# Performance work log

Hardware: AMD Instinct MI355X
Metric: run time of the kernel (lower is better)

## Reference

```python
import jax, jax.numpy as jnp
import numpy as np

NE, NR, D, H, L = 200000, 500, 128, 4, 2
HD = D // H
N, E, B = 32768, 262144, 256
MARGIN = 1.0


def setup_inputs() -> dict:
    key = jax.random.key(0)
    ks = jax.random.split(key, 16)
    nrm = lambda k, shp, s=0.05: jax.random.normal(k, shp, jnp.float32) * s
    inp = {
        'ent_emb': nrm(ks[0], (NE, D)),
        'rel_emb': nrm(ks[1], (NR, D)),
        'rel_prior': nrm(ks[2], (NR, 1)),
    }
    for i, nm in enumerate(['Wq', 'Wk', 'Wv', 'Wo', 'Wek', 'Wev']):
        inp[nm] = nrm(ks[3 + i], (L, D, D))
    for gi, g in enumerate(['h', 't', 'n']):
        kb = jax.random.fold_in(key, 100 + gi)
        k1, k2, k3, k4 = jax.random.split(kb, 4)
        inp[f'x_{g}'] = jax.random.randint(k1, (N,), 0, NE, jnp.int32)
        inp[f'ei_{g}'] = jax.random.randint(k2, (2, E), 0, N, jnp.int32)
        inp[f'ea_{g}'] = jax.random.randint(k3, (E,), 0, NR, jnp.int32)
        inp[f'y_{g}'] = jax.random.randint(k4, (B,), 0, N // B, jnp.int32)
        inp[f's_{g}'] = jnp.full((B,), N // B, dtype=jnp.int32)
    inp['sample'] = jax.random.randint(ks[9], (B, 3), 0, NR, jnp.int32)
    return inp


def gnn_embed(ent_emb, rel_emb, rel_prior, Wq, Wk, Wv, Wo, Wek, Wev, x, ei, ea, y, s):
    n = x.shape[0]
    h = ent_emb[x]                    # [N, D] node features (embedding lookup)
    e_emb = rel_emb[ea]               # [E, D] edge relation embedding
    e_pri = rel_prior[ea]             # [E, 1] scalar relation prior gate
    src, dst = ei[0], ei[1]
    scale = 1.0 / np.sqrt(HD).astype(np.float32)
    for l in range(L):
        q = (h @ Wq[l]).reshape(n, H, HD)[dst]                               # [E,H,HD]
        k = (h @ Wk[l]).reshape(n, H, HD)[src] + (e_emb @ Wek[l]).reshape(-1, H, HD)
        v = (h @ Wv[l]).reshape(n, H, HD)[src] + (e_emb @ Wev[l]).reshape(-1, H, HD)
        score = jnp.sum(q * k, axis=-1) * scale * e_pri                      # [E,H]
        # segment softmax over incoming edges of each destination node
        m = jax.ops.segment_max(score, dst, num_segments=n)
        m = jnp.where(jnp.isfinite(m), m, 0.0)
        ex = jnp.exp(score - m[dst])
        den = jax.ops.segment_sum(ex, dst, num_segments=n)[dst]
        alpha = ex / (den + 1e-16)                                           # [E,H]
        msg = jax.ops.segment_sum((alpha[..., None] * v).reshape(-1, D), dst, num_segments=n)
        h = jax.nn.gelu(h + msg @ Wo[l])                                     # residual + activation
    # get_real_index: exclusive cumsum of graph sizes + local target index
    offsets = jnp.concatenate([jnp.zeros((1,), s.dtype), jnp.cumsum(s)[:-1]])
    return h[offsets + y]             # [B, D]


def reference(ent_emb, rel_emb, rel_prior, Wq, Wk, Wv, Wo, Wek, Wev,
              x_h, ei_h, ea_h, y_h, s_h,
              x_t, ei_t, ea_t, y_t, s_t,
              x_n, ei_n, ea_n, y_n, s_n, sample):
    g = lambda x, ei, ea, y, s: gnn_embed(ent_emb, rel_emb, rel_prior, Wq, Wk, Wv, Wo, Wek, Wev, x, ei, ea, y, s)
    h = g(x_h, ei_h, ea_h, y_h, s_h)[:, None, :]   # [B,1,D]
    t = g(x_t, ei_t, ea_t, y_t, s_t)[:, None, :]
    tn = g(x_n, ei_n, ea_n, y_n, s_n)[:, None, :]
    r = rel_emb[sample[:, 1]][:, None, :]          # [B,1,D]
    proj_t = h + r                                 # TransE projection
    pos = jnp.linalg.norm(t - proj_t + 1e-8, axis=2)   # [B,1]
    negs = jnp.linalg.norm(t - tn + 1e-8, axis=2)      # [B,1]
    neg = jnp.mean(negs, axis=-1)                      # [B]
    # MarginRankingLoss(pos, neg, target=-1): mean(max(0, (pos-neg)+margin)); broadcasts [B,1]-[B] -> [B,B]
    loss = jnp.mean(jnp.maximum(pos - neg + MARGIN, 0.0))
    return loss
```

## Files before the change

### kernel.cpp

```cpp
#include <hip/hip_runtime.h>
#include <hip/hip_bf16.h>
#include <math.h>

#define NEC 200000
#define NRC 500
#define DD 128
#define LLC 2
#define NNODE 32768
#define EEDGE 262144
#define BBATCH 256
#define NG 3
#define BCAP 32

typedef __attribute__((ext_vector_type(8))) short short8;
typedef __attribute__((ext_vector_type(4))) float floatx4;
typedef __attribute__((ext_vector_type(2))) float floatx2;

__device__ __forceinline__ float bf2f(unsigned short u) {
  union { unsigned int i; float f; } c; c.i = ((unsigned int)u) << 16; return c.f;
}
__device__ __forceinline__ unsigned short f2bf(float f) {
  union { float f; unsigned int i; } c; c.f = f;
  unsigned int x = c.i;
  unsigned int r = x + 0x7fffu + ((x >> 16) & 1u);
  return (unsigned short)(r >> 16);
}
__device__ __forceinline__ float bfu_lo(unsigned int u) {
  union { unsigned int i; float f; } c; c.i = u << 16; return c.f;
}
__device__ __forceinline__ float bfu_hi(unsigned int u) {
  union { unsigned int i; float f; } c; c.i = u & 0xffff0000u; return c.f;
}

__device__ __forceinline__ bool detect_fm(const void* ent) {
  unsigned int u = ((const unsigned int*)ent)[threadIdx.x & 63];
  bool big = fabsf(bfu_lo(u)) > 100.f;
  return __ballot(big) != 0ull;
}

__global__ __launch_bounds__(128) void k_prep(const void* ent, const void* rel,
    const void* prior, const void* Wq, const void* Wk, const void* Wv, const void* Wo,
    const void* Wek, const void* Wev,
    float* pris, unsigned short* WT, unsigned short* relk, unsigned short* relv, int* deg) {
  bool fm = detect_fm(ent);
  int bid = blockIdx.x, tid = threadIdx.x;
  if (bid < 4) {
    int r = bid * 128 + tid;
    if (r < NRC) {
      float p = fm ? ((const float*)prior)[r] : bf2f(((const unsigned short*)prior)[r]);
      pris[r] = p * 0.17677669529663687f;
    }
  } else if (bid < 1028) {
    int t = (bid - 4) * 128 + tid;
    int mat = t >> 15;
    int rem = t & 32767;
    int l = rem >> 14;
    int p = rem & 16383;
    int d = p >> 7, c = p & 127;
    const void* W = mat == 0 ? Wq : (mat == 1 ? Wk : (mat == 2 ? Wv : Wo));
    size_t src = (size_t)l * DD * DD + (size_t)c * DD + d;
    float v = fm ? ((const float*)W)[src] : bf2f(((const unsigned short*)W)[src]);
    WT[(((size_t)mat * LLC + l) * DD + d) * DD + c] = f2bf(v);
  } else if (bid < 3028) {
    int rid = bid - 1028;
    int which = rid / 1000;
    int l = (rid / 500) % 2;
    int r = rid % 500;
    int d = tid;
    size_t wofs = (size_t)l * DD * DD;
    const float* Wf = (const float*)(which ? Wev : Wek) + wofs;
    const unsigned short* Wb = (const unsigned short*)(which ? Wev : Wek) + wofs;
    __shared__ float re[DD];
    re[d] = fm ? ((const float*)rel)[r * DD + d] : bf2f(((const unsigned short*)rel)[r * DD + d]);
    __syncthreads();
    float acc = 0.f;
    if (fm) { for (int c = 0; c < DD; ++c) acc += re[c] * Wf[c * DD + d]; }
    else    { for (int c = 0; c < DD; ++c) acc += re[c] * bf2f(Wb[c * DD + d]); }
    unsigned short* out = which ? relv : relk;
    out[((size_t)l * NRC + r) * DD + d] = f2bf(acc);
  } else {
    int t = (bid - 3028) * 128 + tid;
    uint4 z = {0u, 0u, 0u, 0u};
    ((uint4*)deg)[t * 2] = z;
    ((uint4*)deg)[t * 2 + 1] = z;
  }
}

__global__ __launch_bounds__(256) void k_gb(const void* ent,
    const int* x0, const int* x1, const int* x2,
    const int* ei0, const int* ea0, const int* ei1, const int* ea1,
    const int* ei2, const int* ea2,
    unsigned short* hbf, int* deg, unsigned int* bucket) {
  int bid = blockIdx.x, tid = threadIdx.x;
  if (bid < 3072) {
    bool fm = detect_fm(ent);
    int rbase = bid * 32;
    int g = rbase >> 15;
    const int* x = g == 0 ? x0 : (g == 1 ? x1 : x2);
    int c = tid & 31;
    int j4 = tid >> 5;
    int rows[4], xs[4];
    #pragma unroll
    for (int k = 0; k < 4; ++k) {
      rows[k] = rbase + j4 + 8 * k;
      xs[k] = x[rows[k] & (NNODE - 1)];
    }
    if (fm) {
      float4 v[4];
      #pragma unroll
      for (int k = 0; k < 4; ++k)
        v[k] = *reinterpret_cast<const float4*>((const float*)ent + (size_t)xs[k] * DD + c * 4);
      #pragma unroll
      for (int k = 0; k < 4; ++k) {
        uint2 o;
        o.x = ((unsigned int)f2bf(v[k].y) << 16) | (unsigned int)f2bf(v[k].x);
        o.y = ((unsigned int)f2bf(v[k].w) << 16) | (unsigned int)f2bf(v[k].z);
        *reinterpret_cast<uint2*>(hbf + (size_t)rows[k] * DD + c * 4) = o;
      }
    } else {
      uint2 v[4];
      #pragma unroll
      for (int k = 0; k < 4; ++k)
        v[k] = *reinterpret_cast<const uint2*>((const unsigned short*)ent + (size_t)xs[k] * DD + c * 4);
      #pragma unroll
      for (int k = 0; k < 4; ++k)
        *reinterpret_cast<uint2*>(hbf + (size_t)rows[k] * DD + c * 4) = v[k];
    }
  } else {
    int bb = bid - 3072;
    int g = bb >> 8;
    const int* ei = g == 0 ? ei0 : (g == 1 ? ei1 : ei2);
    const int* ea = g == 0 ? ea0 : (g == 1 ? ea1 : ea2);
    int e0 = (bb & 255) * 1024 + tid * 4;
    uint4 d4 = *reinterpret_cast<const uint4*>(ei + EEDGE + e0);
    uint4 s4 = *reinterpret_cast<const uint4*>(ei + e0);
    uint4 r4 = *reinterpret_cast<const uint4*>(ea + e0);
    int* degg = deg + g * NNODE;
    size_t brow = (size_t)g * NNODE;
    #pragma unroll
    for (int k = 0; k < 4; ++k) {
      int dst = (int)((const unsigned int*)&d4)[k];
      unsigned int src = ((const unsigned int*)&s4)[k];
      unsigned int r = ((const unsigned int*)&r4)[k];
      int pos = atomicAdd(&degg[dst], 1);
      if (pos < BCAP)
        bucket[(brow + dst) * BCAP + pos] = src | (r << 15);
    }
  }
}

__device__ __forceinline__ void stage_wt(const unsigned short* WT, int tid,
                                         unsigned short (*Wt)[136]) {
  #pragma unroll
  for (int pass = 0; pass < 8; ++pass) {
    int idx = pass * 256 + tid;
    int d = idx >> 4, c0 = (idx & 15) << 3;
    *reinterpret_cast<short8*>(&Wt[d][c0]) =
        *reinterpret_cast<const short8*>(WT + d * DD + c0);
  }
}

__global__ __launch_bounds__(256) void k_gemm_qkv(const unsigned short* A,
    const unsigned short* WT, int layer, unsigned short* Qo, unsigned char* KV) {
  __shared__ unsigned short Wt[DD][136];
  int mat = blockIdx.y;
  int g = blockIdx.z;
  const unsigned short* Ag = A + (size_t)g * NNODE * DD;
  int tid = threadIdx.x;
  stage_wt(WT + ((size_t)mat * LLC + layer) * DD * DD, tid, Wt);
  __syncthreads();
  int w = tid >> 6, lane = tid & 63;
  int m = lane & 15, quad = lane >> 4;
  int row = blockIdx.x * 64 + w * 16 + m;
  floatx4 acc[8];
  #pragma unroll
  for (int t = 0; t < 8; ++t) acc[t] = (floatx4){0.f, 0.f, 0.f, 0.f};
  const unsigned short* arow = Ag + (size_t)row * DD;
  #pragma unroll
  for (int ks = 0; ks < 4; ++ks) {
    short8 a = *reinterpret_cast<const short8*>(arow + ks * 32 + quad * 8);
    #pragma unroll
    for (int t = 0; t < 8; ++t) {
      short8 b = *reinterpret_cast<const short8*>(&Wt[t * 16 + m][ks * 32 + quad * 8]);
      acc[t] = __builtin_amdgcn_mfma_f32_16x16x32_bf16(a, b, acc[t], 0, 0, 0);
    }
  }
  __syncthreads();
  unsigned short* ut = &Wt[0][0];
  #pragma unroll
  for (int t = 0; t < 8; ++t) {
    #pragma unroll
    for (int r = 0; r < 4; ++r) {
      ut[(w * 16 + quad * 4 + r) * 136 + t * 16 + m] = f2bf(acc[t][r]);
    }
  }
  __syncthreads();
  int rowbase = blockIdx.x * 64;
  if (mat == 0) {
    unsigned short* Og = Qo + (size_t)g * NNODE * DD;
    #pragma unroll
    for (int k = 0; k < 4; ++k) {
      int flat = k * 256 + tid;
      int rw = flat >> 4, c8 = flat & 15;
      short8 v = *reinterpret_cast<const short8*>(ut + rw * 136 + c8 * 8);
      *reinterpret_cast<short8*>(Og + (size_t)(rowbase + rw) * DD + c8 * 8) = v;
    }
  } else {
    unsigned char* kvb = KV + (size_t)g * NNODE * 256 + (mat == 1 ? 0 : 128);
    #pragma unroll
    for (int k = 0; k < 2; ++k) {
      int flat = k * 256 + tid;
      int rw = flat >> 3, c16 = flat & 7;
      const unsigned short* p = ut + rw * 136 + c16 * 16;
      uint4 a = *reinterpret_cast<const uint4*>(p);
      uint4 b = *reinterpret_cast<const uint4*>(p + 8);
      unsigned int w0 = __builtin_amdgcn_cvt_pk_fp8_f32(bfu_lo(a.x), bfu_hi(a.x), 0u, false);
      w0 = __builtin_amdgcn_cvt_pk_fp8_f32(bfu_lo(a.y), bfu_hi(a.y), w0, true);
      unsigned int w1 = __builtin_amdgcn_cvt_pk_fp8_f32(bfu_lo(a.z), bfu_hi(a.z), 0u, false);
      w1 = __builtin_amdgcn_cvt_pk_fp8_f32(bfu_lo(a.w), bfu_hi(a.w), w1, true);
      unsigned int w2 = __builtin_amdgcn_cvt_pk_fp8_f32(bfu_lo(b.x), bfu_hi(b.x), 0u, false);
      w2 = __builtin_amdgcn_cvt_pk_fp8_f32(bfu_lo(b.y), bfu_hi(b.y), w2, true);
      unsigned int w3 = __builtin_amdgcn_cvt_pk_fp8_f32(bfu_lo(b.z), bfu_hi(b.z), 0u, false);
      w3 = __builtin_amdgcn_cvt_pk_fp8_f32(bfu_lo(b.w), bfu_hi(b.w), w3, true);
      uint4 o = {w0, w1, w2, w3};
      *reinterpret_cast<uint4*>(kvb + (size_t)(rowbase + rw) * 256 + c16 * 16) = o;
    }
  }
}

__global__ __launch_bounds__(256) void k_gemm_o(const unsigned short* A,
    const unsigned short* WT, int layer, unsigned short* hbf) {
  __shared__ unsigned short Wt[DD][136];
  int g = blockIdx.y;
  const unsigned short* Ag = A + (size_t)g * NNODE * DD;
  unsigned short* hbg = hbf + (size_t)g * NNODE * DD;
  int tid = threadIdx.x;
  stage_wt(WT + ((size_t)3 * LLC + layer) * DD * DD, tid, Wt);
  __syncthreads();
  int w = tid >> 6, lane = tid & 63;
  int m = lane & 15, quad = lane >> 4;
  int row = blockIdx.x * 64 + w * 16 + m;
  floatx4 acc[8];
  #pragma unroll
  for (int t = 0; t < 8; ++t) acc[t] = (floatx4){0.f, 0.f, 0.f, 0.f};
  const unsigned short* arow = Ag + (size_t)row * DD;
  #pragma unroll
  for (int ks = 0; ks < 4; ++ks) {
    short8 a = *reinterpret_cast<const short8*>(arow + ks * 32 + quad * 8);
    #pragma unroll
    for (int t = 0; t < 8; ++t) {
      short8 b = *reinterpret_cast<const short8*>(&Wt[t * 16 + m][ks * 32 + quad * 8]);
      acc[t] = __builtin_amdgcn_mfma_f32_16x16x32_bf16(a, b, acc[t], 0, 0, 0);
    }
  }
  __syncthreads();
  float* ft = (float*)&Wt[0][0];
  #pragma unroll
  for (int t = 0; t < 8; ++t) {
    #pragma unroll
    for (int r = 0; r < 4; ++r) {
      ft[(w * 16 + quad * 4 + r) * 136 + t * 16 + m] = acc[t][r];
    }
  }
  __syncthreads();
  int rowbase = blockIdx.x * 64;
  #pragma unroll
  for (int k = 0; k < 8; ++k) {
    int flat = k * 256 + tid;
    int rw = flat >> 5, c4 = flat & 31;
    float4 v = *reinterpret_cast<const float4*>(ft + rw * 136 + c4 * 4);
    size_t gi = (size_t)(rowbase + rw) * DD + c4 * 4;
    uint2 hv = *reinterpret_cast<const uint2*>(hbg + gi);
    float h0 = bfu_lo(hv.x), h1 = bfu_hi(hv.x), h2 = bfu_lo(hv.y), h3 = bfu_hi(hv.y);
    float r0, r1, r2, r3;
    {
      float xv = v.x + h0;
      float z2 = 1.5957691216057308f * (xv + 0.044715f * xv * xv * xv);
      r0 = xv / (1.f + __expf(-z2));
      xv = v.y + h1;
      z2 = 1.5957691216057308f * (xv + 0.044715f * xv * xv * xv);
      r1 = xv / (1.f + __expf(-z2));
      xv = v.z + h2;
      z2 = 1.5957691216057308f * (xv + 0.044715f * xv * xv * xv);
      r2 = xv / (1.f + __expf(-z2));
      xv = v.w + h3;
      z2 = 1.5957691216057308f * (xv + 0.044715f * xv * xv * xv);
      r3 = xv / (1.f + __expf(-z2));
    }
    uint2 o;
    o.x = ((unsigned int)f2bf(r1) << 16) | (unsigned int)f2bf(r0);
    o.y = ((unsigned int)f2bf(r3) << 16) | (unsigned int)f2bf(r2);
    *reinterpret_cast<uint2*>(hbg + gi) = o;
  }
}

__global__ __launch_bounds__(256) void k_attn(const unsigned short* Q, const unsigned char* KV,
    const unsigned short* relk, const unsigned short* relv,
    const float* pris, const int* deg, const unsigned int* bucket, int layer,
    unsigned short* msgb) {
  int w = threadIdx.x >> 6, lane = threadIdx.x & 63;
  int half = lane >> 5;
  int hq = (lane >> 4) & 1;
  int sl = lane & 15;
  int g = blockIdx.y;
  int dst = blockIdx.x * 8 + w * 2 + half;
  const unsigned short* rk = relk + (size_t)layer * NRC * DD;
  const unsigned short* rv = relv + (size_t)layer * NRC * DD;
  const unsigned char* KVg = KV + (size_t)g * NNODE * 256;
  size_t gofs = (size_t)g * NNODE * DD;

  uint4 qu = *reinterpret_cast<const uint4*>(Q + gofs + (size_t)dst * DD + sl * 8);
  float q0 = bfu_lo(qu.x), q1 = bfu_hi(qu.x), q2 = bfu_lo(qu.y), q3 = bfu_hi(qu.y);
  float q4 = bfu_lo(qu.z), q5 = bfu_hi(qu.z), q6 = bfu_lo(qu.w), q7 = bfu_hi(qu.w);

  float den = 0.f;
  float m0 = 0.f, m1 = 0.f, m2 = 0.f, m3 = 0.f, m4 = 0.f, m5 = 0.f, m6 = 0.f, m7 = 0.f;
  int dg = deg[g * NNODE + dst]; if (dg > BCAP) dg = BCAP;
  size_t base = ((size_t)g * NNODE + dst) * BCAP;
  if (dg > 0) {
    int niter = (dg + 1) >> 1;
    unsigned int pe = bucket[base + (hq < dg ? hq : dg - 1)];
    for (int i = 0; i < niter; ++i) {
      unsigned int cur = pe;
      int nx = 2 * (i + 1) + hq; if (nx >= dg) nx = dg - 1;
      pe = bucket[base + nx];
      int src = (int)(cur & 32767u);
      int r = (int)(cur >> 15);
      const unsigned char* kvrow = KVg + (size_t)src * 256;
      uint2 k8 = *reinterpret_cast<const uint2*>(kvrow + sl * 8);
      uint2 v8 = *reinterpret_cast<const uint2*>(kvrow + 128 + sl * 8);
      uint4 rku = *reinterpret_cast<const uint4*>(rk + (size_t)r * DD + sl * 8);
      uint4 rvu = *reinterpret_cast<const uint4*>(rv + (size_t)r * DD + sl * 8);
      float p = pris[r];
      floatx2 k01 = __builtin_amdgcn_cvt_pk_f32_fp8(k8.x, false);
      floatx2 k23 = __builtin_amdgcn_cvt_pk_f32_fp8(k8.x, true);
      floatx2 k45 = __builtin_amdgcn_cvt_pk_f32_fp8(k8.y, false);
      floatx2 k67 = __builtin_amdgcn_cvt_pk_f32_fp8(k8.y, true);
      float s = q0 * (k01.x + bfu_lo(rku.x))
              + q1 * (k01.y + bfu_hi(rku.x))
              + q2 * (k23.x + bfu_lo(rku.y))
              + q3 * (k23.y + bfu_hi(rku.y))
              + q4 * (k45.x + bfu_lo(rku.z))
              + q5 * (k45.y + bfu_hi(rku.z))
              + q6 * (k67.x + bfu_lo(rku.w))
              + q7 * (k67.y + bfu_hi(rku.w));
      s += __shfl_xor(s, 1); s += __shfl_xor(s, 2);
      bool valid = (2 * i + hq) < dg;
      float ex = valid ? __expf(s * p) : 0.f;
      floatx2 v01 = __builtin_amdgcn_cvt_pk_f32_fp8(v8.x, false);
      floatx2 v23 = __builtin_amdgcn_cvt_pk_f32_fp8(v8.x, true);
      floatx2 v45 = __builtin_amdgcn_cvt_pk_f32_fp8(v8.y, false);
      floatx2 v67 = __builtin_amdgcn_cvt_pk_f32_fp8(v8.y, true);
      den += ex;
      m0 += ex * (v01.x + bfu_lo(rvu.x));
      m1 += ex * (v01.y + bfu_hi(rvu.x));
      m2 += ex * (v23.x + bfu_lo(rvu.y));
      m3 += ex * (v23.y + bfu_hi(rvu.y));
      m4 += ex * (v45.x + bfu_lo(rvu.z));
      m5 += ex * (v45.y + bfu_hi(rvu.z));
      m6 += ex * (v67.x + bfu_lo(rvu.w));
      m7 += ex * (v67.y + bfu_hi(rvu.w));
    }
  }
  den += __shfl_xor(den, 16);
  m0 += __shfl_xor(m0, 16);
  m1 += __shfl_xor(m1, 16);
  m2 += __shfl_xor(m2, 16);
  m3 += __shfl_xor(m3, 16);
  m4 += __shfl_xor(m4, 16);
  m5 += __shfl_xor(m5, 16);
  m6 += __shfl_xor(m6, 16);
  m7 += __shfl_xor(m7, 16);
  float inv = 1.f / (den + 1e-16f);
  if (hq == 0) {
    uint4 o;
    o.x = ((unsigned int)f2bf(m1 * inv) << 16) | (unsigned int)f2bf(m0 * inv);
    o.y = ((unsigned int)f2bf(m3 * inv) << 16) | (unsigned int)f2bf(m2 * inv);
    o.z = ((unsigned int)f2bf(m5 * inv) << 16) | (unsigned int)f2bf(m4 * inv);
    o.w = ((unsigned int)f2bf(m7 * inv) << 16) | (unsigned int)f2bf(m6 * inv);
    *reinterpret_cast<uint4*>(msgb + gofs + (size_t)dst * DD + sl * 8) = o;
  }
}

__global__ __launch_bounds__(128) void k_ep(const unsigned short* hbf, const void* ent,
    const void* rel,
    const int* y0, const int* s0, const int* y1, const int* s1, const int* y2, const int* s2,
    const int* sample, float* pos, float* neg) {
  bool fm = detect_fm(ent);
  int b = blockIdx.x, d = threadIdx.x;
  int oh = 0, ot = 0, on = 0;
  for (int j = 0; j < b; ++j) { oh += s0[j]; ot += s1[j]; on += s2[j]; }
  int ih = oh + y0[b], it = ot + y1[b], in_ = on + y2[b];
  float th = bf2f(hbf[((size_t)0 * NNODE + ih) * DD + d]);
  float tt = bf2f(hbf[((size_t)1 * NNODE + it) * DD + d]);
  float tn = bf2f(hbf[((size_t)2 * NNODE + in_) * DD + d]);
  int r = sample[b * 3 + 1];
  float rr = fm ? ((const float*)rel)[r * DD + d] : bf2f(((const unsigned short*)rel)[r * DD + d]);
  float dp = tt - (th + rr) + 1e-8f;
  float dn = tt - tn + 1e-8f;
  float ap = dp * dp, an = dn * dn;
  for (int o = 32; o > 0; o >>= 1) { ap += __shfl_down(ap, o); an += __shfl_down(an, o); }
  __shared__ float sa[2], sb[2];
  if ((d & 63) == 0) { sa[d >> 6] = ap; sb[d >> 6] = an; }
  __syncthreads();
  if (d == 0) { pos[b] = sqrtf(sa[0] + sa[1]); neg[b] = sqrtf(sb[0] + sb[1]); }
}

__global__ __launch_bounds__(256) void k_hinge(const float* pos, const float* neg,
    const void* ent, void* out) {
  bool fm = detect_fm(ent);
  __shared__ float ns[BBATCH];
  __shared__ float wsum[4];
  int t = threadIdx.x;
  ns[t] = neg[t];
  float pb = pos[t];
  __syncthreads();
  float local = 0.f;
  for (int j = 0; j < BBATCH; ++j) {
    float v = pb - ns[j] + 1.0f;
    local += v > 0.f ? v : 0.f;
  }
  for (int o = 32; o > 0; o >>= 1) local += __shfl_down(local, o);
  if ((t & 63) == 0) wsum[t >> 6] = local;
  __syncthreads();
  if (t == 0) {
    float loss = (wsum[0] + wsum[1] + wsum[2] + wsum[3]) * (1.f / (256.f * 256.f));
    if (fm) ((float*)out)[0] = loss;
    else    ((unsigned short*)out)[0] = f2bf(loss);
  }
}

extern "C" void kernel_launch(void* const* d_in, const int* in_sizes, int n_in,
                              void* d_out, int out_size, void* d_ws, size_t ws_size,
                              hipStream_t stream) {
  const void* ent   = d_in[0];
  const void* rel   = d_in[1];
  const void* prior = d_in[2];
  const void* Wq  = d_in[3];
  const void* Wk  = d_in[4];
  const void* Wv  = d_in[5];
  const void* Wo  = d_in[6];
  const void* Wek = d_in[7];
  const void* Wev = d_in[8];
  const int* sample = (const int*)d_in[24];

  size_t off = 0;
  char* basep = (char*)d_ws;
  auto alloc = [&](size_t bytes) -> void* {
    void* r = basep + off;
    off = (off + bytes + 255) & ~(size_t)255;
    return r;
  };
  unsigned short* hbf  = (unsigned short*)alloc((size_t)NG * NNODE * DD * 2);
  unsigned short* Qb   = (unsigned short*)alloc((size_t)NG * NNODE * DD * 2);
  unsigned char*  KV   = (unsigned char*)alloc((size_t)NG * NNODE * 256);
  unsigned short* msgb = (unsigned short*)alloc((size_t)NG * NNODE * DD * 2);
  unsigned short* relk = (unsigned short*)alloc((size_t)LLC * NRC * DD * 2);
  unsigned short* relv = (unsigned short*)alloc((size_t)LLC * NRC * DD * 2);
  unsigned short* WT   = (unsigned short*)alloc((size_t)4 * LLC * DD * DD * 2);
  float* pris = (float*)alloc((size_t)NRC * 4);
  int*   deg  = (int*)alloc((size_t)NG * NNODE * 4);
  unsigned int* bucket = (unsigned int*)alloc((size_t)NG * NNODE * BCAP * 4);
  float* pos  = (float*)alloc((size_t)BBATCH * 4);
  float* neg  = (float*)alloc((size_t)BBATCH * 4);

  const int* x0  = (const int*)d_in[9],  *x1 = (const int*)d_in[14], *x2 = (const int*)d_in[19];
  const int* ei0 = (const int*)d_in[10], *ei1 = (const int*)d_in[15], *ei2 = (const int*)d_in[20];
  const int* ea0 = (const int*)d_in[11], *ea1 = (const int*)d_in[16], *ea2 = (const int*)d_in[21];
  const int* y0  = (const int*)d_in[12], *y1 = (const int*)d_in[17], *y2 = (const int*)d_in[22];
  const int* s0  = (const int*)d_in[13], *s1 = (const int*)d_in[18], *s2 = (const int*)d_in[23];

  k_prep<<<3124, 128, 0, stream>>>(ent, rel, prior, Wq, Wk, Wv, Wo, Wek, Wev,
                                   pris, WT, relk, relv, deg);
  k_gb<<<3840, 256, 0, stream>>>(ent, x0, x1, x2, ei0, ea0, ei1, ea1, ei2, ea2,
                                 hbf, deg, bucket);
  for (int l = 0; l < LLC; ++l) {
    k_gemm_qkv<<<dim3(NNODE / 64, 3, NG), 256, 0, stream>>>(hbf, WT, l, Qb, KV);
    k_attn<<<dim3(NNODE / 8, NG), 256, 0, stream>>>(Qb, KV, relk, relv, pris, deg, bucket, l, msgb);
    k_gemm_o<<<dim3(NNODE / 64, NG), 256, 0, stream>>>(msgb, WT, l, hbf);
  }
  k_ep<<<BBATCH, 128, 0, stream>>>(hbf, ent, rel, y0, s0, y1, s1, y2, s2, sample, pos, neg);
  k_hinge<<<1, BBATCH, 0, stream>>>(pos, neg, ent, d_out);
}
```

Before: 471.4 us.

## Replace global-atomic edge bucketing with LDS count, prefix, and place passes

Edge bucketing by destination used to do one global atomicAdd per edge on the degree array. It now runs three passes: 32 sub-blocks per graph count per-node in-degrees with packed 8-bit LDS atomics, a prefix kernel scans those counts into per-block base offsets and degrees, and a place kernel writes bucket slots using LDS atomics plus the base offsets. The embedding gather is split into its own kernel with 8 rows per thread, and degree zeroing is dropped from the prep kernel. This removes contended global atomics, but it adds two extra launches, re-reads the edge list, and the 8-bit packed counters would overflow if one block sees more than 255 edges into a single node.

Result: faster. 460.0 us (-2.4%).

```diff
diff --git a/kernel.cpp b/kernel.cpp
--- a/kernel.cpp
+++ b/kernel.cpp
@@ -11,6 +11,9 @@
 #define BBATCH 256
 #define NG 3
 #define BCAP 32
+#define NSB 32
+#define EPG (EEDGE / NSB)
+#define CNTW (NNODE / 4)
 
 typedef __attribute__((ext_vector_type(8))) short short8;
 typedef __attribute__((ext_vector_type(4))) float floatx4;
@@ -41,7 +44,7 @@
 __global__ __launch_bounds__(128) void k_prep(const void* ent, const void* rel,
     const void* prior, const void* Wq, const void* Wk, const void* Wv, const void* Wo,
     const void* Wek, const void* Wev,
-    float* pris, unsigned short* WT, unsigned short* relk, unsigned short* relv, int* deg) {
+    float* pris, unsigned short* WT, unsigned short* relk, unsigned short* relv) {
   bool fm = detect_fm(ent);
   int bid = blockIdx.x, tid = threadIdx.x;
   if (bid < 4) {
@@ -61,7 +64,7 @@
     size_t src = (size_t)l * DD * DD + (size_t)c * DD + d;
     float v = fm ? ((const float*)W)[src] : bf2f(((const unsigned short*)W)[src]);
     WT[(((size_t)mat * LLC + l) * DD + d) * DD + c] = f2bf(v);
-  } else if (bid < 3028) {
+  } else {
     int rid = bid - 1028;
     int which = rid / 1000;
     int l = (rid / 500) % 2;
@@ -78,74 +81,114 @@
     else    { for (int c = 0; c < DD; ++c) acc += re[c] * bf2f(Wb[c * DD + d]); }
     unsigned short* out = which ? relv : relk;
     out[((size_t)l * NRC + r) * DD + d] = f2bf(acc);
+  }
+}
+
+__global__ __launch_bounds__(256) void k_gather(const void* ent,
+    const int* x0, const int* x1, const int* x2, unsigned short* hbf) {
+  bool fm = detect_fm(ent);
+  int bid = blockIdx.x, tid = threadIdx.x;
+  int rbase = bid * 64;
+  int g = rbase >> 15;
+  const int* x = g == 0 ? x0 : (g == 1 ? x1 : x2);
+  int c = tid & 31;
+  int j8 = tid >> 5;
+  int rows[8], xs[8];
+  #pragma unroll
+  for (int k = 0; k < 8; ++k) {
+    rows[k] = rbase + j8 + 8 * k;
+    xs[k] = x[rows[k] & (NNODE - 1)];
+  }
+  if (fm) {
+    float4 v[8];
+    #pragma unroll
+    for (int k = 0; k < 8; ++k)
+      v[k] = *reinterpret_cast<const float4*>((const float*)ent + (size_t)xs[k] * DD + c * 4);
+    #pragma unroll
+    for (int k = 0; k < 8; ++k) {
+      uint2 o;
+      o.x = ((unsigned int)f2bf(v[k].y) << 16) | (unsigned int)f2bf(v[k].x);
+      o.y = ((unsigned int)f2bf(v[k].w) << 16) | (unsigned int)f2bf(v[k].z);
+      *reinterpret_cast<uint2*>(hbf + (size_t)rows[k] * DD + c * 4) = o;
+    }
   } else {
-    int t = (bid - 3028) * 128 + tid;
-    uint4 z = {0u, 0u, 0u, 0u};
-    ((uint4*)deg)[t * 2] = z;
-    ((uint4*)deg)[t * 2 + 1] = z;
-  }
-}
-
-__global__ __launch_bounds__(256) void k_gb(const void* ent,
-    const int* x0, const int* x1, const int* x2,
-    const int* ei0, const int* ea0, const int* ei1, const int* ea1,
-    const int* ei2, const int* ea2,
-    unsigned short* hbf, int* deg, unsigned int* bucket) {
+    uint2 v[8];
+    #pragma unroll
+    for (int k = 0; k < 8; ++k)
+      v[k] = *reinterpret_cast<const uint2*>((const unsigned short*)ent + (size_t)xs[k] * DD + c * 4);
+    #pragma unroll
+    for (int k = 0; k < 8; ++k)
+      *reinterpret_cast<uint2*>(hbf + (size_t)rows[k] * DD + c * 4) = v[k];
+  }
+}
+
+__global__ __launch_bounds__(1024) void k_count(const int* ei0, const int* ei1,
+    const int* ei2, unsigned int* cntw) {
+  __shared__ unsigned int cnt[CNTW];
   int bid = blockIdx.x, tid = threadIdx.x;
-  if (bid < 3072) {
-    bool fm = detect_fm(ent);
-    int rbase = bid * 32;
-    int g = rbase >> 15;
-    const int* x = g == 0 ? x0 : (g == 1 ? x1 : x2);
-    int c = tid & 31;
-    int j4 = tid >> 5;
-    int rows[4], xs[4];
-    #pragma unroll
-    for (int k = 0; k < 4; ++k) {
-      rows[k] = rbase + j4 + 8 * k;
-      xs[k] = x[rows[k] & (NNODE - 1)];
-    }
-    if (fm) {
-      float4 v[4];
-      #pragma unroll
-      for (int k = 0; k < 4; ++k)
-        v[k] = *reinterpret_cast<const float4*>((const float*)ent + (size_t)xs[k] * DD + c * 4);
-      #pragma unroll
-      for (int k = 0; k < 4; ++k) {
-        uint2 o;
-        o.x = ((unsigned int)f2bf(v[k].y) << 16) | (unsigned int)f2bf(v[k].x);
-        o.y = ((unsigned int)f2bf(v[k].w) << 16) | (unsigned int)f2bf(v[k].z);
-        *reinterpret_cast<uint2*>(hbf + (size_t)rows[k] * DD + c * 4) = o;
-      }
-    } else {
-      uint2 v[4];
-      #pragma unroll
-      for (int k = 0; k < 4; ++k)
-        v[k] = *reinterpret_cast<const uint2*>((const unsigned short*)ent + (size_t)xs[k] * DD + c * 4);
-      #pragma unroll
-      for (int k = 0; k < 4; ++k)
-        *reinterpret_cast<uint2*>(hbf + (size_t)rows[k] * DD + c * 4) = v[k];
-    }
-  } else {
-    int bb = bid - 3072;
-    int g = bb >> 8;
-    const int* ei = g == 0 ? ei0 : (g == 1 ? ei1 : ei2);
-    const int* ea = g == 0 ? ea0 : (g == 1 ? ea1 : ea2);
-    int e0 = (bb & 255) * 1024 + tid * 4;
-    uint4 d4 = *reinterpret_cast<const uint4*>(ei + EEDGE + e0);
-    uint4 s4 = *reinterpret_cast<const uint4*>(ei + e0);
-    uint4 r4 = *reinterpret_cast<const uint4*>(ea + e0);
-    int* degg = deg + g * NNODE;
-    size_t brow = (size_t)g * NNODE;
-    #pragma unroll
-    for (int k = 0; k < 4; ++k) {
-      int dst = (int)((const unsigned int*)&d4)[k];
-      unsigned int src = ((const unsigned int*)&s4)[k];
-      unsigned int r = ((const unsigned int*)&r4)[k];
-      int pos = atomicAdd(&degg[dst], 1);
-      if (pos < BCAP)
-        bucket[(brow + dst) * BCAP + pos] = src | (r << 15);
-    }
+  int g = bid / NSB, grp = bid % NSB;
+  const int* ei = g == 0 ? ei0 : (g == 1 ? ei1 : ei2);
+  #pragma unroll
+  for (int i = 0; i < CNTW / 1024; ++i) cnt[i * 1024 + tid] = 0u;
+  __syncthreads();
+  int e0 = grp * EPG;
+  #pragma unroll
+  for (int i = 0; i < EPG / 1024; ++i) {
+    int dst = ei[EEDGE + e0 + i * 1024 + tid];
+    atomicAdd(&cnt[dst >> 2], 1u << ((dst & 3) * 8));
+  }
+  __syncthreads();
+  unsigned int* out = cntw + (size_t)(g * NSB + grp) * CNTW;
+  #pragma unroll
+  for (int i = 0; i < CNTW / 1024; ++i) out[i * 1024 + tid] = cnt[i * 1024 + tid];
+}
+
+__global__ __launch_bounds__(256) void k_prefix(const unsigned int* cntw,
+    unsigned int* basew, int* deg) {
+  int flat = blockIdx.x * 256 + threadIdx.x;
+  int g = flat / CNTW, wi = flat % CNTW;
+  unsigned int r0 = 0, r1 = 0, r2 = 0, r3 = 0;
+  for (int grp = 0; grp < NSB; ++grp) {
+    size_t idx = (size_t)(g * NSB + grp) * CNTW + wi;
+    unsigned int w = cntw[idx];
+    basew[idx] = r0 | (r1 << 8) | (r2 << 16) | (r3 << 24);
+    r0 += w & 255u; r1 += (w >> 8) & 255u; r2 += (w >> 16) & 255u; r3 += (w >> 24) & 255u;
+  }
+  int4 dv = {(int)r0, (int)r1, (int)r2, (int)r3};
+  *reinterpret_cast<int4*>(deg + (size_t)g * NNODE + wi * 4) = dv;
+}
+
+__global__ __launch_bounds__(1024) void k_place(const int* ei0, const int* ei1,
+    const int* ei2, const int* ea0, const int* ea1, const int* ea2,
+    const unsigned int* basew, unsigned int* bucket) {
+  __shared__ unsigned int cnt[CNTW];
+  __shared__ unsigned int basel[CNTW];
+  int bid = blockIdx.x, tid = threadIdx.x;
+  int g = bid / NSB, grp = bid % NSB;
+  const int* ei = g == 0 ? ei0 : (g == 1 ? ei1 : ei2);
+  const int* ea = g == 0 ? ea0 : (g == 1 ? ea1 : ea2);
+  const unsigned int* brow = basew + (size_t)(g * NSB + grp) * CNTW;
+  #pragma unroll
+  for (int i = 0; i < CNTW / 1024; ++i) {
+    cnt[i * 1024 + tid] = 0u;
+    basel[i * 1024 + tid] = brow[i * 1024 + tid];
+  }
+  __syncthreads();
+  int e0 = grp * EPG;
+  size_t gb = (size_t)g * NNODE;
+  #pragma unroll
+  for (int i = 0; i < EPG / 1024; ++i) {
+    int e = e0 + i * 1024 + tid;
+    int dst = ei[EEDGE + e];
+    unsigned int src = (unsigned int)ei[e];
+    unsigned int r = (unsigned int)ea[e];
+    int sh = (dst & 3) * 8;
+    unsigned int old = atomicAdd(&cnt[dst >> 2], 1u << sh);
+    unsigned int lpos = (old >> sh) & 255u;
+    unsigned int b = (basel[dst >> 2] >> sh) & 255u;
+    unsigned int slot = b + lpos;
+    if (slot < BCAP)
+      bucket[(gb + dst) * BCAP + slot] = src | (r << 15);
   }
 }
 
@@ -461,6 +504,8 @@
   float* pris = (float*)alloc((size_t)NRC * 4);
   int*   deg  = (int*)alloc((size_t)NG * NNODE * 4);
   unsigned int* bucket = (unsigned int*)alloc((size_t)NG * NNODE * BCAP * 4);
+  unsigned int* cntw   = (unsigned int*)alloc((size_t)NG * NSB * CNTW * 4);
+  unsigned int* basew  = (unsigned int*)alloc((size_t)NG * NSB * CNTW * 4);
   float* pos  = (float*)alloc((size_t)BBATCH * 4);
   float* neg  = (float*)alloc((size_t)BBATCH * 4);
 
@@ -470,10 +515,12 @@
   const int* y0  = (const int*)d_in[12], *y1 = (const int*)d_in[17], *y2 = (const int*)d_in[22];
   const int* s0  = (const int*)d_in[13], *s1 = (const int*)d_in[18], *s2 = (const int*)d_in[23];
 
-  k_prep<<<3124, 128, 0, stream>>>(ent, rel, prior, Wq, Wk, Wv, Wo, Wek, Wev,
-                                   pris, WT, relk, relv, deg);
-  k_gb<<<3840, 256, 0, stream>>>(ent, x0, x1, x2, ei0, ea0, ei1, ea1, ei2, ea2,
-                                 hbf, deg, bucket);
+  k_prep<<<3028, 128, 0, stream>>>(ent, rel, prior, Wq, Wk, Wv, Wo, Wek, Wev,
+                                   pris, WT, relk, relv);
+  k_gather<<<1536, 256, 0, stream>>>(ent, x0, x1, x2, hbf);
+  k_count<<<NG * NSB, 1024, 0, stream>>>(ei0, ei1, ei2, cntw);
+  k_prefix<<<NG * CNTW / 256, 256, 0, stream>>>(cntw, basew, deg);
+  k_place<<<NG * NSB, 1024, 0, stream>>>(ei0, ei1, ei2, ea0, ea1, ea2, basew, bucket);
   for (int l = 0; l < LLC; ++l) {
     k_gemm_qkv<<<dim3(NNODE / 64, 3, NG), 256, 0, stream>>>(hbf, WT, l, Qb, KV);
     k_attn<<<dim3(NNODE / 8, NG), 256, 0, stream>>>(Qb, KV, relk, relv, pris, deg, bucket, l, msgb);
```
